# Optimization experiments

Measured on AMD Instinct MI355X. Metric: run time of the kernel, lower is better.

Reference implementation:

```python
import jax, jax.numpy as jnp
import numpy as np

NEG_PENALTY = 0.03
B, C, L = 64, 2048, 1024


def setup_inputs() -> dict:
    key = jax.random.key(0)
    k1, k2, k3 = jax.random.split(key, 3)
    ranks = jax.random.normal(k1, (B, C), dtype=jnp.float32)
    labels = jax.random.randint(k2, (B, C), 0, 2, dtype=jnp.int32)
    class_ids_loaded = jnp.sort(jax.random.randint(k3, (L,), 0, C, dtype=jnp.int64))
    return {"ranks": ranks, "labels": labels, "class_ids_loaded": class_ids_loaded}


def reference(ranks, labels, class_ids_loaded):
    # Gather the loaded classes: [B, L]
    r = ranks[:, class_ids_loaded]
    lab = labels[:, class_ids_loaded]
    pos = (lab == 1).astype(r.dtype)   # correct-class mask
    neg = (lab != 1).astype(r.dtype)   # absent-class mask (neg_labels == 1)
    # Pairwise hinge: relu(neg_penalty + wrong - correct), c along axis 1, w along axis 2
    pen = jax.nn.relu(NEG_PENALTY + r[:, None, :] - r[:, :, None])  # [B, L, L]
    # Mask to (correct, wrong) pairs and reduce; average over batch
    loss = jnp.einsum('bcw,bc,bw->', pen, pos, neg) / r.shape[0]
    return loss.reshape(1)
```

## Files before the change

kernel.cpp:

```cpp
#include <hip/hip_runtime.h>

#define B 64
#define C 2048
#define L 1024
#define WCHUNK 256
#define NBLK_W (L / WCHUNK)

__global__ void zero_kernel(float* __restrict__ out) {
    out[0] = 0.0f;
}

__global__ __launch_bounds__(1024)
void RankingLoss_kernel(const float* __restrict__ ranks,
                        const int* __restrict__ labels,
                        const int* __restrict__ ids,
                        float* __restrict__ out)
{
    __shared__ float s_r[L];
    __shared__ float s_neg[L];
    __shared__ float s_partial[16];

    const int b  = blockIdx.x / NBLK_W;
    const int wc = blockIdx.x % NBLK_W;
    const int t  = threadIdx.x;

    {
        const int id  = ids[t];
        const float r = ranks[b * C + id];
        const int lab = labels[b * C + id];
        s_r[t]   = r;
        s_neg[t] = (lab != 1) ? 1.0f : 0.0f;
    }
    __syncthreads();

    const float rc   = s_r[t];
    const float posc = 1.0f - s_neg[t];

    float acc = 0.0f;
    if (posc != 0.0f) {
        const int w0 = wc * WCHUNK;
        const float base = 0.03f - rc;
        #pragma unroll 8
        for (int i = 0; i < WCHUNK; ++i) {
            const int w = w0 + i;
            const float v = base + s_r[w];
            acc += s_neg[w] * fmaxf(v, 0.0f);
        }
    }

    #pragma unroll
    for (int off = 32; off > 0; off >>= 1)
        acc += __shfl_down(acc, off, 64);

    const int lane = t & 63;
    const int wave = t >> 6;
    if (lane == 0) s_partial[wave] = acc;
    __syncthreads();

    if (wave == 0) {
        float v = (lane < 16) ? s_partial[lane] : 0.0f;
        #pragma unroll
        for (int off = 8; off > 0; off >>= 1)
            v += __shfl_down(v, off, 64);
        if (lane == 0)
            atomicAdd(out, v * (1.0f / B));
    }
}

extern "C" void kernel_launch(void* const* d_in, const int* in_sizes, int n_in,
                              void* d_out, int out_size, void* d_ws, size_t ws_size,
                              hipStream_t stream) {
    const float* ranks = (const float*)d_in[0];
    const int* labels  = (const int*)d_in[1];
    const int* ids     = (const int*)d_in[2];
    float* out         = (float*)d_out;

    zero_kernel<<<1, 1, 0, stream>>>(out);

    RankingLoss_kernel<<<B * NBLK_W, 1024, 0, stream>>>(ranks, labels, ids, out);
}
```

Before: 66.49 us.

## Encode masks as sentinel values and register-tile four correct classes per thread

Positive and negative masks are folded into the rank values themselves: wrong-class slots hold -1e30 for positives and correct-class slots hold +1e30 for negatives, so the relu zeroes masked pairs without a multiply or branch. Each thread now handles four correct classes against a 64-wide wrong sub-chunk, using float4 LDS reads and reusing each loaded value across four accumulators. This removes divergence from the old per-thread positive check and cuts shared-memory traffic per pair, at the cost of doing the arithmetic for masked pairs too. It depends on the sentinels never overflowing or producing NaNs.

```diff
diff --git a/kernel.cpp b/kernel.cpp
--- a/kernel.cpp
+++ b/kernel.cpp
@@ -5,6 +5,8 @@
 #define L 1024
 #define WCHUNK 256
 #define NBLK_W (L / WCHUNK)
+#define NC 4
+#define WSUB 64
 
 __global__ void zero_kernel(float* __restrict__ out) {
     out[0] = 0.0f;
@@ -16,8 +18,8 @@
                         const int* __restrict__ ids,
                         float* __restrict__ out)
 {
-    __shared__ float s_r[L];
-    __shared__ float s_neg[L];
+    __shared__ float s_rw[L];
+    __shared__ float s_rc[L];
     __shared__ float s_partial[16];
 
     const int b  = blockIdx.x / NBLK_W;
@@ -28,42 +30,53 @@
         const int id  = ids[t];
         const float r = ranks[b * C + id];
         const int lab = labels[b * C + id];
-        s_r[t]   = r;
-        s_neg[t] = (lab != 1) ? 1.0f : 0.0f;
+        const bool pos = (lab == 1);
+        s_rw[t] = pos ? -1e30f : r;
+        s_rc[t] = pos ? r : 1e30f;
     }
     __syncthreads();
 
-    const float rc   = s_r[t];
-    const float posc = 1.0f - s_neg[t];
+    const int i = t & 255;
+    const int j = t >> 8;
 
-    float acc = 0.0f;
-    if (posc != 0.0f) {
-        const int w0 = wc * WCHUNK;
-        const float base = 0.03f - rc;
-        #pragma unroll 8
-        for (int i = 0; i < WCHUNK; ++i) {
-            const int w = w0 + i;
-            const float v = base + s_r[w];
-            acc += s_neg[w] * fmaxf(v, 0.0f);
+    float base[NC];
+    #pragma unroll
+    for (int k = 0; k < NC; ++k)
+        base[k] = 0.03f - s_rc[i + 256 * k];
+
+    float acc[NC] = {0.f, 0.f, 0.f, 0.f};
+    const int w0 = wc * WCHUNK + j * WSUB;
+
+    #pragma unroll 4
+    for (int it = 0; it < WSUB / 4; ++it) {
+        const float4 rw = *(const float4*)&s_rw[w0 + it * 4];
+        #pragma unroll
+        for (int k = 0; k < NC; ++k) {
+            acc[k] += fmaxf(rw.x + base[k], 0.0f);
+            acc[k] += fmaxf(rw.y + base[k], 0.0f);
+            acc[k] += fmaxf(rw.z + base[k], 0.0f);
+            acc[k] += fmaxf(rw.w + base[k], 0.0f);
         }
     }
 
+    float v = (acc[0] + acc[1]) + (acc[2] + acc[3]);
+
     #pragma unroll
     for (int off = 32; off > 0; off >>= 1)
-        acc += __shfl_down(acc, off, 64);
+        v += __shfl_down(v, off, 64);
 
     const int lane = t & 63;
     const int wave = t >> 6;
-    if (lane == 0) s_partial[wave] = acc;
+    if (lane == 0) s_partial[wave] = v;
     __syncthreads();
 
     if (wave == 0) {
-        float v = (lane < 16) ? s_partial[lane] : 0.0f;
+        float s = (lane < 16) ? s_partial[lane] : 0.0f;
         #pragma unroll
         for (int off = 8; off > 0; off >>= 1)
-            v += __shfl_down(v, off, 64);
+            s += __shfl_down(s, off, 64);
         if (lane == 0)
-            atomicAdd(out, v * (1.0f / B));
+            atomicAdd(out, s * (1.0f / B));
     }
 }
 
@@ -76,6 +89,5 @@
     float* out         = (float*)d_out;
 
     zero_kernel<<<1, 1, 0, stream>>>(out);
-
     RankingLoss_kernel<<<B * NBLK_W, 1024, 0, stream>>>(ranks, labels, ids, out);
 }
```

After: 65.97 us. About the same (-0.8%).
